# Optimization experiments

Measured on AMD Instinct MI355X. Metric: run time of the kernel, lower is better.

The kernel has to match this reference:

```python
import jax, jax.numpy as jnp
import numpy as np

B, S, H = 32, 512, 512
L, NHW, WIDTH = 2, 2, 3
IN = H * (WIDTH + 1)  # 2048


def setup_inputs() -> dict:
    key = jax.random.key(0)
    ks = jax.random.split(key, 11)
    sd = 1.0 / np.sqrt(H)
    return {
        "inputs": jax.random.normal(ks[0], (B, S, H), jnp.float32),
        "fwd_pad": jax.random.normal(ks[1], (L, WIDTH, H), jnp.float32) * sd,
        "bwd_pad": jax.random.normal(ks[2], (L, WIDTH, H), jnp.float32) * sd,
        "fwd_w": jax.random.normal(ks[3], (L, H, IN), jnp.float32) * (1.0 / np.sqrt(IN)),
        "fwd_b": jax.random.normal(ks[4], (L, H), jnp.float32) * 0.01,
        "bwd_w": jax.random.normal(ks[5], (L, H, IN), jnp.float32) * (1.0 / np.sqrt(IN)),
        "bwd_b": jax.random.normal(ks[6], (L, H), jnp.float32) * 0.01,
        "fwd_hw_w": jax.random.normal(ks[7], (L, NHW, 2 * H, H), jnp.float32) * sd,
        "fwd_hw_b": jax.random.normal(ks[8], (L, NHW, 2 * H), jnp.float32) * 0.01,
        "bwd_hw_w": jax.random.normal(ks[9], (L, NHW, 2 * H, H), jnp.float32) * sd,
        "bwd_hw_b": jax.random.normal(ks[10], (L, NHW, 2 * H), jnp.float32) * 0.01,
    }


def _highway(x, hw_w, hw_b):
    # AllenNLP Highway: per layer Linear(H, 2H); split -> (nonlinear, gate)
    for j in range(NHW):
        proj = jnp.einsum("bsh,gh->bsg", x, hw_w[j]) + hw_b[j]
        nonlin, gate = jnp.split(proj, 2, axis=-1)
        g = jax.nn.sigmoid(gate)
        x = g * x + (1.0 - g) * jax.nn.relu(nonlin)
    return x


def reference(inputs, fwd_pad, bwd_pad, fwd_w, fwd_b, bwd_w, bwd_b,
              fwd_hw_w, fwd_hw_b, bwd_hw_w, bwd_hw_b):
    b, s, h = inputs.shape
    idx = jnp.arange(s)[:, None] + jnp.arange(WIDTH + 1)[None, :]  # [S, W+1]
    xf, xb = inputs, inputs
    layers = []
    for i in range(L):
        pad_f = jnp.broadcast_to(fwd_pad[i], (b, WIDTH, h))
        pad_b = jnp.broadcast_to(bwd_pad[i], (b, WIDTH, h))
        padded_f = jnp.concatenate([pad_f, xf, pad_b], axis=1)  # [B, S+2W, H]
        padded_b = jnp.concatenate([pad_f, xb, pad_b], axis=1)
        # forward windows: start..start+W ; backward windows: start+W..start+2W
        win_f = padded_f[:, idx].reshape(b, s, IN)
        win_b = padded_b[:, idx + WIDTH].reshape(b, s, IN)
        hf = jax.nn.relu(jnp.einsum("bsk,hk->bsh", win_f, fwd_w[i]) + fwd_b[i])
        hb = jax.nn.relu(jnp.einsum("bsk,hk->bsh", win_b, bwd_w[i]) + bwd_b[i])
        xf = _highway(hf, fwd_hw_w[i], fwd_hw_b[i])
        xb = _highway(hb, bwd_hw_w[i], bwd_hw_b[i])
        layers.append(jnp.concatenate([xf, xb], axis=-1))
    return jnp.stack(layers, axis=0)  # [L, B, S, 2H]
```

## Files before the change

kernel.cpp:

```cpp
#include <hip/hip_runtime.h>


typedef __attribute__((ext_vector_type(8))) _Float16 h8;
typedef __attribute__((ext_vector_type(4))) float f4;

#define AS1(p) ((__attribute__((address_space(1))) void*)(p))
#define AS3(p) ((__attribute__((address_space(3))) void*)(p))

__global__ void cvt_kernel(const float* __restrict__ in, _Float16* __restrict__ out, int n) {
  int i = (blockIdx.x * blockDim.x + threadIdx.x) * 4;
  if (i >= n) return;
  float4 v = *reinterpret_cast<const float4*>(in + i);
  union { _Float16 h[4]; unsigned long long u; } p;
  p.h[0] = (_Float16)v.x; p.h[1] = (_Float16)v.y;
  p.h[2] = (_Float16)v.z; p.h[3] = (_Float16)v.w;
  *reinterpret_cast<unsigned long long*>(out + i) = p.u;
}

__global__ __launch_bounds__(256, 2) void conv_kernel(
    const _Float16* __restrict__ xinF, const _Float16* __restrict__ xinB,
    const _Float16* __restrict__ wF,   const _Float16* __restrict__ wB,
    const float* __restrict__ biasF,   const float* __restrict__ biasB,
    const _Float16* __restrict__ padF, const _Float16* __restrict__ padB,
    _Float16* __restrict__ xoutF,      _Float16* __restrict__ xoutB)
{
  const int dir = blockIdx.z;
  const _Float16* xin  = dir ? xinB  : xinF;
  const _Float16* wgt  = dir ? wB    : wF;
  const float*    bias = dir ? biasB : biasF;
  _Float16*       xout = dir ? xoutB : xoutF;
  const int tof = dir ? 3 : 0;

  const int n0 = blockIdx.x << 7;
  const int m0 = blockIdx.y << 7;
  const int b  = m0 >> 9;
  const int s0 = m0 & 511;

  __shared__ char smem[32768];
  char* smA = smem;
  char* smB = smem + 16384;

  const int tid  = threadIdx.x;
  const int lane = tid & 63;
  const int wv   = tid >> 6;
  const int wm   = wv >> 1, wn = wv & 1;
  const int r15  = lane & 15, rk = lane >> 4;
  const int swz  = (r15 & 7) << 4;

  f4 acc[4][4] = {};

  for (int kt = 0; kt < 32; ++kt) {
    const int kbase = kt << 6;
    __syncthreads();
    #pragma unroll
    for (int i = 0; i < 4; ++i) {
      const int c   = (i << 8) + tid;
      const int row = c >> 3;
      const int cbs = ((c & 7) << 4) ^ ((row & 7) << 4);
      const int kg  = kbase + (cbs >> 1);
      const int t   = s0 + row + tof + (kg >> 9);
      const int hh  = kg & 511;
      const _Float16* src;
      if (t < 3)        src = padF + t * 512 + hh;
      else if (t < 515) src = xin + ((((size_t)(b << 9)) + (t - 3)) << 9) + hh;
      else              src = padB + (t - 515) * 512 + hh;
      char* dst = smA + (((i << 8) + (tid & 192)) << 4);
      __builtin_amdgcn_global_load_lds(AS1(src), AS3(dst), 16, 0, 0);
    }
    #pragma unroll
    for (int i = 0; i < 4; ++i) {
      const int c   = (i << 8) + tid;
      const int row = c >> 3;
      const int cbs = ((c & 7) << 4) ^ ((row & 7) << 4);
      const _Float16* src = wgt + (((size_t)(n0 + row)) << 11) + kbase + (cbs >> 1);
      char* dst = smB + (((i << 8) + (tid & 192)) << 4);
      __builtin_amdgcn_global_load_lds(AS1(src), AS3(dst), 16, 0, 0);
    }
    asm volatile("s_waitcnt vmcnt(0)" ::: "memory");
    __syncthreads();
    #pragma unroll
    for (int kk = 0; kk < 2; ++kk) {
      h8 av[4], bv[4];
      #pragma unroll
      for (int mi = 0; mi < 4; ++mi) {
        const int row = (wm << 6) + (mi << 4) + r15;
        av[mi] = *reinterpret_cast<const h8*>(smA + row * 128 + (((kk << 6) + (rk << 4)) ^ swz));
      }
      #pragma unroll
      for (int ni = 0; ni < 4; ++ni) {
        const int row = (wn << 6) + (ni << 4) + r15;
        bv[ni] = *reinterpret_cast<const h8*>(smB + row * 128 + (((kk << 6) + (rk << 4)) ^ swz));
      }
      #pragma unroll
      for (int mi = 0; mi < 4; ++mi)
        #pragma unroll
        for (int ni = 0; ni < 4; ++ni)
          acc[mi][ni] = __builtin_amdgcn_mfma_f32_16x16x32_f16(av[mi], bv[ni], acc[mi][ni], 0, 0, 0);
    }
  }

  #pragma unroll
  for (int ni = 0; ni < 4; ++ni) {
    const int col = n0 + (wn << 6) + (ni << 4) + r15;
    const float bb = bias[col];
    #pragma unroll
    for (int mi = 0; mi < 4; ++mi) {
      const int mr = m0 + (wm << 6) + (mi << 4) + (rk << 2);
      #pragma unroll
      for (int r = 0; r < 4; ++r) {
        float v = acc[mi][ni][r] + bb;
        v = fmaxf(v, 0.f);
        xout[(((size_t)(mr + r)) << 9) + col] = (_Float16)v;
      }
    }
  }
}

__global__ __launch_bounds__(256, 2) void hw_kernel(
    const _Float16* __restrict__ xinF, const _Float16* __restrict__ xinB,
    const _Float16* __restrict__ wF,   const _Float16* __restrict__ wB,
    const float* __restrict__ hbF,     const float* __restrict__ hbB,
    _Float16* __restrict__ xoutF,      _Float16* __restrict__ xoutB,
    float* __restrict__ outF,          float* __restrict__ outB,
    const int write_out)
{
  const int dir = blockIdx.z;
  const _Float16* xin = dir ? xinB : xinF;
  const _Float16* wgt = dir ? wB   : wF;
  const float*    hb  = dir ? hbB  : hbF;
  _Float16*      xout = dir ? xoutB : xoutF;
  float*         outp = dir ? outB  : outF;

  const int n0 = blockIdx.x << 7;
  const int m0 = blockIdx.y << 7;

  __shared__ char smem[49152];
  char* smA = smem;
  char* smN = smem + 16384;
  char* smG = smem + 32768;

  const int tid  = threadIdx.x;
  const int lane = tid & 63;
  const int wv   = tid >> 6;
  const int wm   = wv >> 1, wn = wv & 1;
  const int r15  = lane & 15, rk = lane >> 4;
  const int swz  = (r15 & 7) << 4;

  f4 an[4][4] = {};
  f4 ag[4][4] = {};

  for (int kt = 0; kt < 8; ++kt) {
    const int kbase = kt << 6;
    __syncthreads();
    #pragma unroll
    for (int i = 0; i < 4; ++i) {
      const int c    = (i << 8) + tid;
      const int row  = c >> 3;
      const int cbs  = ((c & 7) << 4) ^ ((row & 7) << 4);
      const int kof  = kbase + (cbs >> 1);
      const int dsto = (((i << 8) + (tid & 192)) << 4);
      __builtin_amdgcn_global_load_lds(AS1(xin + (((size_t)(m0 + row)) << 9) + kof), AS3(smA + dsto), 16, 0, 0);
      __builtin_amdgcn_global_load_lds(AS1(wgt + (((size_t)(n0 + row)) << 9) + kof), AS3(smN + dsto), 16, 0, 0);
      __builtin_amdgcn_global_load_lds(AS1(wgt + (((size_t)(512 + n0 + row)) << 9) + kof), AS3(smG + dsto), 16, 0, 0);
    }
    asm volatile("s_waitcnt vmcnt(0)" ::: "memory");
    __syncthreads();
    #pragma unroll
    for (int kk = 0; kk < 2; ++kk) {
      h8 av[4], nv[4], gv[4];
      #pragma unroll
      for (int mi = 0; mi < 4; ++mi) {
        const int row = (wm << 6) + (mi << 4) + r15;
        av[mi] = *reinterpret_cast<const h8*>(smA + row * 128 + (((kk << 6) + (rk << 4)) ^ swz));
      }
      #pragma unroll
      for (int ni = 0; ni < 4; ++ni) {
        const int row = (wn << 6) + (ni << 4) + r15;
        const int o = row * 128 + (((kk << 6) + (rk << 4)) ^ swz);
        nv[ni] = *reinterpret_cast<const h8*>(smN + o);
        gv[ni] = *reinterpret_cast<const h8*>(smG + o);
      }
      #pragma unroll
      for (int mi = 0; mi < 4; ++mi)
        #pragma unroll
        for (int ni = 0; ni < 4; ++ni) {
          an[mi][ni] = __builtin_amdgcn_mfma_f32_16x16x32_f16(av[mi], nv[ni], an[mi][ni], 0, 0, 0);
          ag[mi][ni] = __builtin_amdgcn_mfma_f32_16x16x32_f16(av[mi], gv[ni], ag[mi][ni], 0, 0, 0);
        }
    }
  }

  #pragma unroll
  for (int ni = 0; ni < 4; ++ni) {
    const int col = n0 + (wn << 6) + (ni << 4) + r15;
    const float bn = hb[col];
    const float bg = hb[512 + col];
    #pragma unroll
    for (int mi = 0; mi < 4; ++mi) {
      const int mr = m0 + (wm << 6) + (mi << 4) + (rk << 2);
      #pragma unroll
      for (int r = 0; r < 4; ++r) {
        const size_t m = (size_t)(mr + r);
        const float xo = (float)xin[(m << 9) + col];
        const float nl = fmaxf(an[mi][ni][r] + bn, 0.f);
        const float gt = ag[mi][ni][r] + bg;
        const float g  = 1.f / (1.f + __expf(-gt));
        const float xn = g * xo + (1.f - g) * nl;
        xout[(m << 9) + col] = (_Float16)xn;
        if (write_out) outp[m * 1024 + col] = xn;
      }
    }
  }
}

extern "C" void kernel_launch(void* const* d_in, const int* in_sizes, int n_in,
                              void* d_out, int out_size, void* d_ws, size_t ws_size,
                              hipStream_t stream) {
  (void)in_sizes; (void)n_in; (void)out_size; (void)ws_size;
  const float* inputs   = (const float*)d_in[0];
  const float* fwd_pad  = (const float*)d_in[1];
  const float* bwd_pad  = (const float*)d_in[2];
  const float* fwd_w    = (const float*)d_in[3];
  const float* fwd_b    = (const float*)d_in[4];
  const float* bwd_w    = (const float*)d_in[5];
  const float* bwd_b    = (const float*)d_in[6];
  const float* fwd_hw_w = (const float*)d_in[7];
  const float* fwd_hw_b = (const float*)d_in[8];
  const float* bwd_hw_w = (const float*)d_in[9];
  const float* bwd_hw_b = (const float*)d_in[10];
  float* out = (float*)d_out;

  _Float16* ws = (_Float16*)d_ws;
  size_t off = 0;
  auto alloc = [&](size_t n) { _Float16* p = ws + off; off += n; return p; };
  const size_t MH = (size_t)16384 * 512;
  _Float16* in_h = alloc(MH);
  _Float16* xAf  = alloc(MH);
  _Float16* xBf  = alloc(MH);
  _Float16* xAb  = alloc(MH);
  _Float16* xBb  = alloc(MH);
  _Float16* cwF  = alloc((size_t)2 * 512 * 2048);
  _Float16* cwB  = alloc((size_t)2 * 512 * 2048);
  _Float16* hwF  = alloc((size_t)2 * 2 * 1024 * 512);
  _Float16* hwB  = alloc((size_t)2 * 2 * 1024 * 512);
  _Float16* pF   = alloc(2 * 3 * 512);
  _Float16* pB   = alloc(2 * 3 * 512);

  auto cvt = [&](const float* s, _Float16* d, int n) {
    cvt_kernel<<<dim3(n >> 10), dim3(256), 0, stream>>>(s, d, n);
  };
  cvt(inputs,   in_h, 1 << 23);
  cvt(fwd_w,    cwF,  1 << 21);
  cvt(bwd_w,    cwB,  1 << 21);
  cvt(fwd_hw_w, hwF,  1 << 21);
  cvt(bwd_hw_w, hwB,  1 << 21);
  cvt(fwd_pad,  pF,   3072);
  cvt(bwd_pad,  pB,   3072);

  _Float16* curF = in_h;
  _Float16* curB = in_h;
  _Float16* pingF = xAf; _Float16* pongF = xBf;
  _Float16* pingB = xAb; _Float16* pongB = xBb;

  for (int l = 0; l < 2; ++l) {
    conv_kernel<<<dim3(4, 128, 2), dim3(256), 0, stream>>>(
        curF, curB,
        cwF + (size_t)l * 512 * 2048, cwB + (size_t)l * 512 * 2048,
        fwd_b + l * 512, bwd_b + l * 512,
        pF + l * 1536, pB + l * 1536,
        pingF, pingB);
    for (int j = 0; j < 2; ++j) {
      const _Float16* hinF = (j == 0) ? pingF : pongF;
      const _Float16* hinB = (j == 0) ? pingB : pongB;
      _Float16* houtF = (j == 0) ? pongF : pingF;
      _Float16* houtB = (j == 0) ? pongB : pingB;
      hw_kernel<<<dim3(4, 128, 2), dim3(256), 0, stream>>>(
          hinF, hinB,
          hwF + (size_t)(l * 2 + j) * 1024 * 512, hwB + (size_t)(l * 2 + j) * 1024 * 512,
          fwd_hw_b + (l * 2 + j) * 1024, bwd_hw_b + (l * 2 + j) * 1024,
          houtF, houtB,
          out + (size_t)l * 16384 * 1024, out + (size_t)l * 16384 * 1024 + 512,
          (j == 1) ? 1 : 0);
    }
    curF = pingF; curB = pingB;
    _Float16* t;
    t = pingF; pingF = pongF; pongF = t;
    t = pingB; pingB = pongB; pongB = t;
  }
}
```

Baseline: 621.5 us.

## Double-buffer LDS, enlarge tiles to 512 threads, swizzle block order for conv and highway

Both GEMM kernels move to 512-thread blocks with 256-row M tiles (conv also takes a 256-wide N tile) and use 128 KB of LDS. That LDS holds double-buffered A/B stages, so the next K tile is fetched by global_load_lds while the current one is computed, with a partial vmcnt wait. The 3D grid is flattened into a 1D grid with an XCD-style block swizzle, and the conv K order is permuted, both to improve L2 locality. MFMA sections are wrapped in s_setprio. The large LDS use limits occupancy to one block per CU and adds register pressure from the bigger accumulator arrays.

```diff
diff --git a/kernel.cpp b/kernel.cpp
--- a/kernel.cpp
+++ b/kernel.cpp
@@ -17,95 +17,123 @@
   *reinterpret_cast<unsigned long long*>(out + i) = p.u;
 }
 
-__global__ __launch_bounds__(256, 2) void conv_kernel(
+__global__ __launch_bounds__(512, 2) void conv_kernel(
     const _Float16* __restrict__ xinF, const _Float16* __restrict__ xinB,
     const _Float16* __restrict__ wF,   const _Float16* __restrict__ wB,
     const float* __restrict__ biasF,   const float* __restrict__ biasB,
     const _Float16* __restrict__ padF, const _Float16* __restrict__ padB,
     _Float16* __restrict__ xoutF,      _Float16* __restrict__ xoutB)
 {
-  const int dir = blockIdx.z;
+  const int bid = blockIdx.x;
+  const int swzb = ((bid & 7) << 5) + (bid >> 3);
+  const int nblk = swzb & 1;
+  const int mblk = (swzb >> 1) & 63;
+  const int dir  = swzb >> 7;
+
   const _Float16* xin  = dir ? xinB  : xinF;
   const _Float16* wgt  = dir ? wB    : wF;
   const float*    bias = dir ? biasB : biasF;
   _Float16*       xout = dir ? xoutB : xoutF;
   const int tof = dir ? 3 : 0;
 
-  const int n0 = blockIdx.x << 7;
-  const int m0 = blockIdx.y << 7;
+  const int n0 = nblk << 8;
+  const int m0 = mblk << 8;
   const int b  = m0 >> 9;
   const int s0 = m0 & 511;
 
-  __shared__ char smem[32768];
-  char* smA = smem;
-  char* smB = smem + 16384;
+  __shared__ char smem[131072];
+  char* A0 = smem;
+  char* A1 = smem + 32768;
+  char* Bu0 = smem + 65536;
+  char* Bu1 = smem + 98304;
 
   const int tid  = threadIdx.x;
   const int lane = tid & 63;
   const int wv   = tid >> 6;
-  const int wm   = wv >> 1, wn = wv & 1;
+  const int wm   = wv >> 2, wn = wv & 3;
   const int r15  = lane & 15, rk = lane >> 4;
-  const int swz  = (r15 & 7) << 4;
-
-  f4 acc[4][4] = {};
-
-  for (int kt = 0; kt < 32; ++kt) {
+  const int swzk = (r15 & 7) << 4;
+
+  f4 acc[8][4] = {};
+
+  auto STAGE = [&](char* sA, char* sB, int t) {
+    const int kt = ((t & 3) << 3) | (t >> 2);
     const int kbase = kt << 6;
-    __syncthreads();
     #pragma unroll
     for (int i = 0; i < 4; ++i) {
-      const int c   = (i << 8) + tid;
+      const int c   = (i << 9) + tid;
       const int row = c >> 3;
       const int cbs = ((c & 7) << 4) ^ ((row & 7) << 4);
       const int kg  = kbase + (cbs >> 1);
-      const int t   = s0 + row + tof + (kg >> 9);
+      const int tr  = s0 + row + tof + (kg >> 9);
       const int hh  = kg & 511;
       const _Float16* src;
-      if (t < 3)        src = padF + t * 512 + hh;
-      else if (t < 515) src = xin + ((((size_t)(b << 9)) + (t - 3)) << 9) + hh;
-      else              src = padB + (t - 515) * 512 + hh;
-      char* dst = smA + (((i << 8) + (tid & 192)) << 4);
+      if (tr < 3)        src = padF + tr * 512 + hh;
+      else if (tr < 515) src = xin + ((((size_t)(b << 9)) + (tr - 3)) << 9) + hh;
+      else               src = padB + (tr - 515) * 512 + hh;
+      char* dst = sA + (((i << 9) + (tid & 448)) << 4);
       __builtin_amdgcn_global_load_lds(AS1(src), AS3(dst), 16, 0, 0);
     }
     #pragma unroll
     for (int i = 0; i < 4; ++i) {
-      const int c   = (i << 8) + tid;
+      const int c   = (i << 9) + tid;
       const int row = c >> 3;
       const int cbs = ((c & 7) << 4) ^ ((row & 7) << 4);
       const _Float16* src = wgt + (((size_t)(n0 + row)) << 11) + kbase + (cbs >> 1);
-      char* dst = smB + (((i << 8) + (tid & 192)) << 4);
+      char* dst = sB + (((i << 9) + (tid & 448)) << 4);
       __builtin_amdgcn_global_load_lds(AS1(src), AS3(dst), 16, 0, 0);
     }
-    asm volatile("s_waitcnt vmcnt(0)" ::: "memory");
-    __syncthreads();
+  };
+
+  auto COMPUTE = [&](char* sA, char* sB) {
     #pragma unroll
     for (int kk = 0; kk < 2; ++kk) {
-      h8 av[4], bv[4];
-      #pragma unroll
-      for (int mi = 0; mi < 4; ++mi) {
-        const int row = (wm << 6) + (mi << 4) + r15;
-        av[mi] = *reinterpret_cast<const h8*>(smA + row * 128 + (((kk << 6) + (rk << 4)) ^ swz));
+      h8 av[8], bv[4];
+      #pragma unroll
+      for (int mi = 0; mi < 8; ++mi) {
+        const int row = (wm << 7) + (mi << 4) + r15;
+        av[mi] = *reinterpret_cast<const h8*>(sA + row * 128 + (((kk << 6) + (rk << 4)) ^ swzk));
       }
       #pragma unroll
       for (int ni = 0; ni < 4; ++ni) {
         const int row = (wn << 6) + (ni << 4) + r15;
-        bv[ni] = *reinterpret_cast<const h8*>(smB + row * 128 + (((kk << 6) + (rk << 4)) ^ swz));
-      }
-      #pragma unroll
-      for (int mi = 0; mi < 4; ++mi)
+        bv[ni] = *reinterpret_cast<const h8*>(sB + row * 128 + (((kk << 6) + (rk << 4)) ^ swzk));
+      }
+      __builtin_amdgcn_s_setprio(1);
+      #pragma unroll
+      for (int mi = 0; mi < 8; ++mi)
         #pragma unroll
         for (int ni = 0; ni < 4; ++ni)
           acc[mi][ni] = __builtin_amdgcn_mfma_f32_16x16x32_f16(av[mi], bv[ni], acc[mi][ni], 0, 0, 0);
-    }
-  }
+      __builtin_amdgcn_s_setprio(0);
+    }
+  };
+
+  STAGE(A0, Bu0, 0);
+  for (int t = 0; t < 31; ++t) {
+    char* cA = (t & 1) ? A1 : A0;
+    char* cB = (t & 1) ? Bu1 : Bu0;
+    char* nA = (t & 1) ? A0 : A1;
+    char* nB = (t & 1) ? Bu0 : Bu1;
+    __builtin_amdgcn_s_barrier();
+    STAGE(nA, nB, t + 1);
+    asm volatile("s_waitcnt vmcnt(8)" ::: "memory");
+    __builtin_amdgcn_s_barrier();
+    asm volatile("" ::: "memory");
+    COMPUTE(cA, cB);
+  }
+  asm volatile("s_waitcnt vmcnt(0)" ::: "memory");
+  __builtin_amdgcn_s_barrier();
+  asm volatile("" ::: "memory");
+  COMPUTE(A1, Bu1);
 
   #pragma unroll
   for (int ni = 0; ni < 4; ++ni) {
     const int col = n0 + (wn << 6) + (ni << 4) + r15;
     const float bb = bias[col];
     #pragma unroll
-    for (int mi = 0; mi < 4; ++mi) {
-      const int mr = m0 + (wm << 6) + (mi << 4) + (rk << 2);
+    for (int mi = 0; mi < 8; ++mi) {
+      const int mr = m0 + (wm << 7) + (mi << 4) + (rk << 2);
       #pragma unroll
       for (int r = 0; r < 4; ++r) {
         float v = acc[mi][ni][r] + bb;
@@ -116,7 +144,7 @@
   }
 }
 
-__global__ __launch_bounds__(256, 2) void hw_kernel(
+__global__ __launch_bounds__(512, 2) void hw_kernel(
     const _Float16* __restrict__ xinF, const _Float16* __restrict__ xinB,
     const _Float16* __restrict__ wF,   const _Float16* __restrict__ wB,
     const float* __restrict__ hbF,     const float* __restrict__ hbB,
@@ -124,62 +152,72 @@
     float* __restrict__ outF,          float* __restrict__ outB,
     const int write_out)
 {
-  const int dir = blockIdx.z;
+  const int bid = blockIdx.x;
+  const int swzb = ((bid & 7) << 6) + (bid >> 3);
+  const int nblk = swzb & 3;
+  const int mblk = (swzb >> 2) & 63;
+  const int dir  = swzb >> 8;
+
   const _Float16* xin = dir ? xinB : xinF;
   const _Float16* wgt = dir ? wB   : wF;
   const float*    hb  = dir ? hbB  : hbF;
   _Float16*      xout = dir ? xoutB : xoutF;
   float*         outp = dir ? outB  : outF;
 
-  const int n0 = blockIdx.x << 7;
-  const int m0 = blockIdx.y << 7;
-
-  __shared__ char smem[49152];
-  char* smA = smem;
-  char* smN = smem + 16384;
-  char* smG = smem + 32768;
+  const int n0 = nblk << 7;
+  const int m0 = mblk << 8;
+
+  __shared__ char smem[131072];
+  char* A0 = smem;
+  char* A1 = smem + 32768;
+  char* Bu0 = smem + 65536;
+  char* Bu1 = smem + 98304;
 
   const int tid  = threadIdx.x;
   const int lane = tid & 63;
   const int wv   = tid >> 6;
   const int wm   = wv >> 1, wn = wv & 1;
   const int r15  = lane & 15, rk = lane >> 4;
-  const int swz  = (r15 & 7) << 4;
+  const int swzk = (r15 & 7) << 4;
 
   f4 an[4][4] = {};
   f4 ag[4][4] = {};
 
-  for (int kt = 0; kt < 8; ++kt) {
-    const int kbase = kt << 6;
-    __syncthreads();
+  auto STAGE = [&](char* sA, char* sB, int t) {
+    const int kbase = t << 6;
     #pragma unroll
     for (int i = 0; i < 4; ++i) {
-      const int c    = (i << 8) + tid;
-      const int row  = c >> 3;
-      const int cbs  = ((c & 7) << 4) ^ ((row & 7) << 4);
-      const int kof  = kbase + (cbs >> 1);
-      const int dsto = (((i << 8) + (tid & 192)) << 4);
-      __builtin_amdgcn_global_load_lds(AS1(xin + (((size_t)(m0 + row)) << 9) + kof), AS3(smA + dsto), 16, 0, 0);
-      __builtin_amdgcn_global_load_lds(AS1(wgt + (((size_t)(n0 + row)) << 9) + kof), AS3(smN + dsto), 16, 0, 0);
-      __builtin_amdgcn_global_load_lds(AS1(wgt + (((size_t)(512 + n0 + row)) << 9) + kof), AS3(smG + dsto), 16, 0, 0);
-    }
-    asm volatile("s_waitcnt vmcnt(0)" ::: "memory");
-    __syncthreads();
+      const int c   = (i << 9) + tid;
+      const int row = c >> 3;
+      const int cbs = ((c & 7) << 4) ^ ((row & 7) << 4);
+      const int kof = kbase + (cbs >> 1);
+      char* dstA = sA + (((i << 9) + (tid & 448)) << 4);
+      __builtin_amdgcn_global_load_lds(AS1(xin + (((size_t)(m0 + row)) << 9) + kof),
+                                       AS3(dstA), 16, 0, 0);
+      const int grow = n0 + (row & 127) + ((row >> 7) << 9);
+      char* dstB = sB + (((i << 9) + (tid & 448)) << 4);
+      __builtin_amdgcn_global_load_lds(AS1(wgt + (((size_t)grow) << 9) + kof),
+                                       AS3(dstB), 16, 0, 0);
+    }
+  };
+
+  auto COMPUTE = [&](char* sA, char* sB) {
     #pragma unroll
     for (int kk = 0; kk < 2; ++kk) {
       h8 av[4], nv[4], gv[4];
       #pragma unroll
       for (int mi = 0; mi < 4; ++mi) {
         const int row = (wm << 6) + (mi << 4) + r15;
-        av[mi] = *reinterpret_cast<const h8*>(smA + row * 128 + (((kk << 6) + (rk << 4)) ^ swz));
+        av[mi] = *reinterpret_cast<const h8*>(sA + row * 128 + (((kk << 6) + (rk << 4)) ^ swzk));
       }
       #pragma unroll
       for (int ni = 0; ni < 4; ++ni) {
-        const int row = (wn << 6) + (ni << 4) + r15;
-        const int o = row * 128 + (((kk << 6) + (rk << 4)) ^ swz);
-        nv[ni] = *reinterpret_cast<const h8*>(smN + o);
-        gv[ni] = *reinterpret_cast<const h8*>(smG + o);
-      }
+        const int rowN = (wn << 6) + (ni << 4) + r15;
+        const int cb = (((kk << 6) + (rk << 4)) ^ swzk);
+        nv[ni] = *reinterpret_cast<const h8*>(sB + rowN * 128 + cb);
+        gv[ni] = *reinterpret_cast<const h8*>(sB + (128 + rowN) * 128 + cb);
+      }
+      __builtin_amdgcn_s_setprio(1);
       #pragma unroll
       for (int mi = 0; mi < 4; ++mi)
         #pragma unroll
@@ -187,8 +225,27 @@
           an[mi][ni] = __builtin_amdgcn_mfma_f32_16x16x32_f16(av[mi], nv[ni], an[mi][ni], 0, 0, 0);
           ag[mi][ni] = __builtin_amdgcn_mfma_f32_16x16x32_f16(av[mi], gv[ni], ag[mi][ni], 0, 0, 0);
         }
-    }
-  }
+      __builtin_amdgcn_s_setprio(0);
+    }
+  };
+
+  STAGE(A0, Bu0, 0);
+  for (int t = 0; t < 7; ++t) {
+    char* cA = (t & 1) ? A1 : A0;
+    char* cB = (t & 1) ? Bu1 : Bu0;
+    char* nA = (t & 1) ? A0 : A1;
+    char* nB = (t & 1) ? Bu0 : Bu1;
+    __builtin_amdgcn_s_barrier();
+    STAGE(nA, nB, t + 1);
+    asm volatile("s_waitcnt vmcnt(8)" ::: "memory");
+    __builtin_amdgcn_s_barrier();
+    asm volatile("" ::: "memory");
+    COMPUTE(cA, cB);
+  }
+  asm volatile("s_waitcnt vmcnt(0)" ::: "memory");
+  __builtin_amdgcn_s_barrier();
+  asm volatile("" ::: "memory");
+  COMPUTE(A1, Bu1);
 
   #pragma unroll
   for (int ni = 0; ni < 4; ++ni) {
@@ -263,7 +320,7 @@
   _Float16* pingB = xAb; _Float16* pongB = xBb;
 
   for (int l = 0; l < 2; ++l) {
-    conv_kernel<<<dim3(4, 128, 2), dim3(256), 0, stream>>>(
+    conv_kernel<<<dim3(256), dim3(512), 0, stream>>>(
         curF, curB,
         cwF + (size_t)l * 512 * 2048, cwB + (size_t)l * 512 * 2048,
         fwd_b + l * 512, bwd_b + l * 512,
@@ -274,7 +331,7 @@
       const _Float16* hinB = (j == 0) ? pingB : pongB;
       _Float16* houtF = (j == 0) ? pongF : pingF;
       _Float16* houtB = (j == 0) ? pongB : pingB;
-      hw_kernel<<<dim3(4, 128, 2), dim3(256), 0, stream>>>(
+      hw_kernel<<<dim3(512), dim3(512), 0, stream>>>(
           hinF, hinB,
           hwF + (size_t)(l * 2 + j) * 1024 * 512, hwB + (size_t)(l * 2 + j) * 1024 * 512,
           fwd_hw_b + (l * 2 + j) * 1024, bwd_hw_b + (l * 2 + j) * 1024,
```

Result: no change. 615.1 us (-1.0%).
